# Kernel tuning notes

Hardware: AMD Instinct MI355X
Metric: run time of the kernel (lower is better)

## Reference

```python
import jax, jax.numpy as jnp
import numpy as np

INPUT_DIM = 512
SMOOTH_FACTOR = 1.0
NOISE_THRESHOLD = 0.0
TAIL_THRESHOLD = 0.45


def setup_inputs() -> dict:
    key = jax.random.key(0)
    k1, k2, k3, k4, k5 = jax.random.split(key, 5)
    B, T, D = 16, 4096, INPUT_DIM
    hidden = jax.random.normal(k1, (B, T, D), dtype=jnp.float32)
    mask = jnp.ones((B, 1, T), dtype=jnp.float32)
    # Conv1d(D, D, kernel=3) weight [out, in, k], Linear(D, 1) weight [1, D]
    conv_w = jax.random.normal(k2, (D, D, 3), dtype=jnp.float32) * (1.0 / np.sqrt(D * 3))
    conv_b = jax.random.normal(k3, (D,), dtype=jnp.float32) * 0.01
    out_w = jax.random.normal(k4, (1, D), dtype=jnp.float32) * (1.0 / np.sqrt(D))
    out_b = jax.random.normal(k5, (1,), dtype=jnp.float32) * 0.01
    return dict(hidden=hidden, mask=mask, conv_w=conv_w, conv_b=conv_b,
                out_w=out_w, out_b=out_b)


def _cif(hidden, alphas):
    """Vectorized continuous integrate-and-fire.
    hidden: [B, T1, D], alphas: [B, T1] -> padded frames [B, T1, D].
    Equivalent to the torch boolean-mask gather/roll/scatter version: for the
    k-th fire at time t_k, frame_k = Q[t_k] - Q[t_{k-1}] where
    Q[t] = cumsum(alpha*h)[t] - frac(cumsum(alpha))[t] * h[t].
    """
    B, T1, D = hidden.shape
    ps = jnp.cumsum(alphas, axis=1)                      # prefix sum of alphas
    psf = jnp.floor(ps)
    prev_psf = jnp.concatenate([jnp.zeros((B, 1), psf.dtype), psf[:, :-1]], axis=1)
    fire = (psf - prev_psf) > 0                          # [B, T1] bool, fire indicator
    frac = ps - psf                                      # remains at each position
    P = jnp.cumsum(alphas[..., None] * hidden, axis=1)   # [B, T1, D]
    Q = P - frac[..., None] * hidden                     # boundary-adjusted prefix
    k = jnp.cumsum(fire.astype(jnp.int32), axis=1) - 1   # fire ordinal per position
    idx = jnp.where(fire, k, T1)                         # dump non-fires to extra slot
    upd = jnp.where(fire[..., None], Q, 0.0)
    Qs = jnp.zeros((B, T1 + 1, D), hidden.dtype).at[jnp.arange(B)[:, None], idx].add(upd)[:, :T1]
    frames = Qs - jnp.concatenate([jnp.zeros((B, 1, D), hidden.dtype), Qs[:, :-1]], axis=1)
    batch_len = fire.sum(axis=1)                         # number of fires per batch
    valid = jnp.arange(T1)[None, :] < batch_len[:, None]
    return jnp.where(valid[..., None], frames, 0.0)


def reference(hidden, mask, conv_w, conv_b, out_w, out_b):
    B, T, D = hidden.shape
    # conv over time with pad (l_order=1, r_order=1), kernel 3, then ReLU
    x = jnp.transpose(hidden, (0, 2, 1))                 # [B, D, T]
    y = jax.lax.conv_general_dilated(x, conv_w, (1,), [(1, 1)],
                                     dimension_numbers=('NCH', 'OIH', 'NCH'))
    y = jax.nn.relu(y + conv_b[None, :, None])
    y = jnp.transpose(y, (0, 2, 1))                      # [B, T, D]
    o = y @ out_w.T + out_b                              # [B, T, 1]
    alphas = jax.nn.relu(jax.nn.sigmoid(o) * SMOOTH_FACTOR - NOISE_THRESHOLD)
    mk = jnp.transpose(mask, (0, 2, 1))                  # [B, T, 1]
    alphas = (alphas * mk)[..., 0]                       # [B, T]
    mk2 = mk[..., 0]                                     # [B, T]
    # tail_process_fn: add tail_threshold at first padded position
    zeros_t = jnp.zeros((B, 1), alphas.dtype)
    ones_t = jnp.ones((B, 1), alphas.dtype)
    mask_1 = jnp.concatenate([mk2, zeros_t], axis=1)     # [B, T+1]
    mask_2 = jnp.concatenate([ones_t, mk2], axis=1)
    tail = (mask_2 - mask_1) * TAIL_THRESHOLD
    alphas = jnp.concatenate([alphas, zeros_t], axis=1) + tail   # [B, T+1]
    h = jnp.concatenate([hidden, jnp.zeros((B, 1, D), hidden.dtype)], axis=1)
    token_num = jnp.floor(alphas.sum(-1))                # [B]
    acoustic = _cif(h, alphas)                           # [B, T+1, D] zero-padded
    # data-dependent truncation (eager, matches torch .item())
    token_num_int = int(np.asarray(jnp.max(token_num)).astype(np.int32))
    acoustic = acoustic[:, :token_num_int, :]
    return acoustic, token_num, alphas
```

## Files before the change

### kernel.cpp

```cpp
#include <hip/hip_runtime.h>
#include <math.h>

#define B_ 16
#define T_ 4096
#define D_ 512
#define T1_ 4097
#define NTHR 1024

#define SMOOTH_FACTOR 1.0
#define NOISE_THRESHOLD 0.0
#define TAIL_THRESHOLD 0.45

typedef short bf16x8 __attribute__((ext_vector_type(8)));
typedef float f32x16 __attribute__((ext_vector_type(16)));
union U4 { uint4 u; bf16x8 s; };

#define WB_OFF   ((size_t)0)
#define A64_OFF  ((size_t)3145728)
#define FT_OFF   ((size_t)3670144)
#define FF_OFF   ((size_t)3932352)
#define LEN_OFF  ((size_t)4456768)

__device__ __forceinline__ unsigned bf_rne(unsigned x) {
    return (x + 0x7FFFu + ((x >> 16) & 1u)) >> 16;
}

__global__ void k_wt(const float* __restrict__ cw, uint4* __restrict__ wb) {
    int idx = blockIdx.x * 256 + threadIdx.x;
    if (idx >= 196608) return;
    int o  = idx & 511;
    int r  = idx >> 9;
    int kg = r & 1;
    int rc = r >> 1;
    int comp = rc / 96;
    int c    = rc - comp * 96;
    unsigned uw[4];
    #pragma unroll
    for (int j = 0; j < 4; ++j) {
        unsigned short us[2];
        #pragma unroll
        for (int q = 0; q < 2; ++q) {
            int e = j * 2 + q;
            int k = c * 16 + kg * 8 + e;
            int tap = k >> 9, i = k & 511;
            float v = cw[((size_t)o * D_ + i) * 3 + tap];
            unsigned x  = __float_as_uint(v);
            unsigned hi = bf_rne(x);
            if (comp == 0) us[q] = (unsigned short)hi;
            else {
                float rem = v - __uint_as_float(hi << 16);
                us[q] = (unsigned short)bf_rne(__float_as_uint(rem));
            }
        }
        uw[j] = (unsigned)us[0] | ((unsigned)us[1] << 16);
    }
    wb[idx] = make_uint4(uw[0], uw[1], uw[2], uw[3]);
}

__global__ __launch_bounds__(NTHR)
void k_conv(const float* __restrict__ h, const uint4* __restrict__ wb,
            const float* __restrict__ cbp, const float* __restrict__ owp,
            const float* __restrict__ mask, const float* __restrict__ obp,
            float* __restrict__ out_alpha, double* __restrict__ a64) {
    extern __shared__ uint4 lds[];
    uint4* Ahi = lds;
    uint4* Ami = lds + 66 * 65;

    const int tid  = threadIdx.x;
    const int b    = blockIdx.y;
    const int t0   = blockIdx.x * 64;
    const int lane = tid & 63;
    const int w    = tid >> 6;
    const int l31  = lane & 31;
    const int kg   = lane >> 5;

    const float* hb = h + (size_t)b * T_ * D_;

    {
        float4 x0, x1, y0, y1;
        int idx = tid;
        if (idx < 4224) {
            int r = idx >> 6, cu4 = idx & 63, t = t0 - 1 + r;
            if (t >= 0 && t < T_) {
                const float* p = hb + (size_t)t * D_ + cu4 * 8;
                x0 = *(const float4*)p; x1 = *(const float4*)(p + 4);
            } else { x0 = x1 = make_float4(0.f, 0.f, 0.f, 0.f); }
        }
        for (int it = 0; it < 5; ++it) {
            int nidx = idx + 1024;
            if (it < 4 && nidx < 4224) {
                int r = nidx >> 6, cu4 = nidx & 63, t = t0 - 1 + r;
                if (t >= 0 && t < T_) {
                    const float* p = hb + (size_t)t * D_ + cu4 * 8;
                    y0 = *(const float4*)p; y1 = *(const float4*)(p + 4);
                } else { y0 = y1 = make_float4(0.f, 0.f, 0.f, 0.f); }
            }
            if (idx < 4224) {
                float v[8] = {x0.x, x0.y, x0.z, x0.w, x1.x, x1.y, x1.z, x1.w};
                unsigned hw[4], mw[4];
                #pragma unroll
                for (int j = 0; j < 4; ++j) {
                    unsigned short hs_[2], ms_[2];
                    #pragma unroll
                    for (int q = 0; q < 2; ++q) {
                        float f = v[j * 2 + q];
                        unsigned hi = bf_rne(__float_as_uint(f));
                        float rem = f - __uint_as_float(hi << 16);
                        hs_[q] = (unsigned short)hi;
                        ms_[q] = (unsigned short)bf_rne(__float_as_uint(rem));
                    }
                    hw[j] = hs_[0] | ((unsigned)hs_[1] << 16);
                    mw[j] = ms_[0] | ((unsigned)ms_[1] << 16);
                }
                int r = idx >> 6, cu4 = idx & 63;
                Ahi[r * 65 + cu4] = make_uint4(hw[0], hw[1], hw[2], hw[3]);
                Ami[r * 65 + cu4] = make_uint4(mw[0], mw[1], mw[2], mw[3]);
            }
            x0 = y0; x1 = y1; idx = nidx;
        }
    }
    __syncthreads();

    f32x16 acc0 = {0,0,0,0,0,0,0,0,0,0,0,0,0,0,0,0};
    f32x16 acc1 = acc0;

    const uint4* wph = wb + ((size_t)kg * 512 + w * 32 + l31);
    const uint4* wpm = wph + 98304;

    U4 whA, wmA, whB, wmB;
    U4 ah0A, am0A, ah1A, am1A, ah0B, am0B, ah1B, am1B;

    #define LOADW(Q, WH, WM) {                 \
        size_t c_ = (size_t)(Q) * 1024;        \
        WH.u = wph[c_];  WM.u = wpm[c_]; }

    #define LOADA(Q, AH0, AM0, AH1, AM1) {                              \
        int ia_ = (l31 + ((Q) >> 5)) * 65 + (((Q) & 31) << 1) + kg;     \
        AH0.u = Ahi[ia_];            AM0.u = Ami[ia_];                  \
        AH1.u = Ahi[ia_ + 32 * 65];  AM1.u = Ami[ia_ + 32 * 65]; }

    #define MF3(AH, AM, CC, WH, WM) {                                           \
        CC = __builtin_amdgcn_mfma_f32_32x32x16_bf16(AH.s, WH.s, CC, 0, 0, 0);  \
        CC = __builtin_amdgcn_mfma_f32_32x32x16_bf16(AH.s, WM.s, CC, 0, 0, 0);  \
        CC = __builtin_amdgcn_mfma_f32_32x32x16_bf16(AM.s, WH.s, CC, 0, 0, 0); }

    LOADW(0, whA, wmA);
    LOADW(1, whB, wmB);
    LOADA(0, ah0A, am0A, ah1A, am1A);

    for (int q = 0; q < 96; q += 2) {
        LOADA(q + 1, ah0B, am0B, ah1B, am1B);
        MF3(ah0A, am0A, acc0, whA, wmA);
        MF3(ah1A, am1A, acc1, whA, wmA);
        if (q + 2 < 96) {
            LOADW(q + 2, whA, wmA);
            LOADA(q + 2, ah0A, am0A, ah1A, am1A);
        }
        MF3(ah0B, am0B, acc0, whB, wmB);
        MF3(ah1B, am1B, acc1, whB, wmB);
        if (q + 3 < 96) LOADW(q + 3, whB, wmB);
    }
    #undef LOADW
    #undef LOADA
    #undef MF3

    const int o = w * 32 + l31;
    const double cbv = (double)cbp[o];
    const double owv = (double)owp[o];
    __syncthreads();
    double* pw = (double*)lds;

    #pragma unroll
    for (int s = 0; s < 2; ++s) {
        const f32x16 ac = s ? acc1 : acc0;
        #pragma unroll
        for (int v = 0; v < 16; ++v) {
            double z = (double)ac[v] + cbv;
            z = z > 0.0 ? z : 0.0;
            double p = owv * z;
            #pragma unroll
            for (int off = 1; off < 32; off <<= 1) p += __shfl_xor(p, off);
            if (l31 == 0) {
                int m = (v & 3) + 8 * (v >> 2) + 4 * kg;
                pw[w * 64 + s * 32 + m] = p;
            }
        }
    }
    __syncthreads();

    if (tid < 64) {
        int t = t0 + tid;
        double osum = (double)obp[0];
        #pragma unroll
        for (int j = 0; j < 16; ++j) osum += pw[j * 64 + tid];
        double sg = 1.0 / (1.0 + exp(-osum));
        double ap = sg * SMOOTH_FACTOR - NOISE_THRESHOLD;
        if (ap < 0.0) ap = 0.0;
        double mk = (double)mask[b * T_ + t];
        double mprev = (t == 0) ? 1.0 : (double)mask[b * T_ + t - 1];
        double a = ap * mk + TAIL_THRESHOLD * (mprev - mk);
        out_alpha[(size_t)b * T1_ + t] = (float)a;
        a64[(size_t)b * T1_ + t] = a;
    }
}

__global__ void k_scan(const double* __restrict__ a64, const float* __restrict__ mask,
                       float* __restrict__ out_tok, float* __restrict__ out_alpha,
                       int* __restrict__ fire_t, double* __restrict__ fire_frac,
                       int* __restrict__ blen) {
    const int b = blockIdx.x;
    const int lane = threadIdx.x;
    const double* ab = a64 + (size_t)b * T1_;
    double carry = 0.0;
    int nf = 0;

    double a = ab[lane];
    for (int c = 0; c < 65; ++c) {
        int t = c * 64 + lane;
        if (t == T_) {
            a = TAIL_THRESHOLD * (double)mask[b * T_ + T_ - 1];
            out_alpha[(size_t)b * T1_ + T_] = (float)a;
        } else if (t > T_) {
            a = 0.0;
        }
        int tn = t + 64;
        double anext = (tn < T_) ? ab[tn] : 0.0;
        double x = a;
        #pragma unroll
        for (int off = 1; off < 64; off <<= 1) {
            double y = __shfl_up(x, off);
            if (lane >= off) x += y;
        }
        double ps = carry + x;
        double ps_prev = __shfl_up(ps, 1);
        if (lane == 0) ps_prev = carry;
        double psf = floor(ps), ppsf = floor(ps_prev);
        bool fire = (t <= T_) && (psf > ppsf);
        unsigned long long m = __ballot(fire);
        if (fire) {
            int k = nf + (int)__popcll(m & ((1ull << lane) - 1ull));
            fire_t[(size_t)b * T1_ + k] = t;
            fire_frac[(size_t)b * T1_ + k] = ps - psf;
        }
        nf += (int)__popcll(m);
        carry = __shfl(ps, 63);
        a = anext;
    }
    if (lane == 0) {
        blen[b] = nf;
        out_tok[b] = (float)floor(carry);
    }
}

__global__ void k_frames(const float* __restrict__ h, const double* __restrict__ a64,
                         const int* __restrict__ fire_t, const double* __restrict__ fire_frac,
                         const int* __restrict__ blen, float* __restrict__ out, int K) {
    const int k = blockIdx.x;
    const int b = blockIdx.y;
    const int tid = threadIdx.x;
    double ax = 0.0, ay = 0.0, az = 0.0, aw = 0.0;
    const int len = blen[b];
    if (k < len) {
        const int t1 = fire_t[(size_t)b * T1_ + k];
        const int t0 = (k > 0) ? fire_t[(size_t)b * T1_ + k - 1] : -1;
        const double f1 = fire_frac[(size_t)b * T1_ + k];
        const double f0 = (k > 0) ? fire_frac[(size_t)b * T1_ + k - 1] : 0.0;
        if (t0 >= 0 && t0 < T_) {
            float4 hv = *(const float4*)(h + ((size_t)b * T_ + t0) * D_ + (tid << 2));
            ax = fma(f0, (double)hv.x, ax); ay = fma(f0, (double)hv.y, ay);
            az = fma(f0, (double)hv.z, az); aw = fma(f0, (double)hv.w, aw);
        }
        for (int t = t0 + 1; t <= t1; ++t) {
            if (t >= T_) break;
            double c = a64[(size_t)b * T1_ + t] - ((t == t1) ? f1 : 0.0);
            float4 hv = *(const float4*)(h + ((size_t)b * T_ + t) * D_ + (tid << 2));
            ax = fma(c, (double)hv.x, ax); ay = fma(c, (double)hv.y, ay);
            az = fma(c, (double)hv.z, az); aw = fma(c, (double)hv.w, aw);
        }
    }
    float4 o = make_float4((float)ax, (float)ay, (float)az, (float)aw);
    *(float4*)(out + ((size_t)b * K + k) * D_ + (tid << 2)) = o;
}

extern "C" void kernel_launch(void* const* d_in, const int* in_sizes, int n_in,
                              void* d_out, int out_size, void* d_ws, size_t ws_size,
                              hipStream_t stream) {
    const float* h    = (const float*)d_in[0];
    const float* mask = (const float*)d_in[1];
    const float* cw   = (const float*)d_in[2];
    const float* cb   = (const float*)d_in[3];
    const float* ow   = (const float*)d_in[4];
    const float* ob   = (const float*)d_in[5];

    char* ws = (char*)d_ws;
    uint4*  wb        = (uint4*)(ws + WB_OFF);
    double* a64       = (double*)(ws + A64_OFF);
    int*    fire_t    = (int*)(ws + FT_OFF);
    double* fire_frac = (double*)(ws + FF_OFF);
    int*    blen      = (int*)(ws + LEN_OFF);

    long long K = ((long long)out_size - B_ - (long long)B_ * T1_) / ((long long)B_ * D_);
    if (K < 1) K = 1;
    float* out_ac    = (float*)d_out;
    float* out_tok   = out_ac + (size_t)B_ * K * D_;
    float* out_alpha = out_tok + B_;

    const int lds = 2 * 66 * 65 * 16;
    (void)hipFuncSetAttribute((const void*)k_conv,
                              hipFuncAttributeMaxDynamicSharedMemorySize, lds);

    k_wt<<<dim3(768), dim3(256), 0, stream>>>(cw, wb);
    k_conv<<<dim3(T_ / 64, B_), dim3(NTHR), lds, stream>>>(h, wb, cb, ow, mask, ob,
                                                           out_alpha, a64);
    k_scan<<<dim3(B_), dim3(64), 0, stream>>>(a64, mask, out_tok, out_alpha,
                                              fire_t, fire_frac, blen);
    k_frames<<<dim3((unsigned)K, B_), dim3(128), 0, stream>>>(h, a64, fire_t, fire_frac,
                                                              blen, out_ac, (int)K);
}
```

Measured before the change: 416.6 us.

## Enlarge conv tile to 128 timesteps with 2x2 warp tiling and staged channel halves

Each conv block now covers 128 timesteps instead of 64. The 16 waves are arranged as 8 output groups by 2 time groups, and each wave computes a 2x2 set of 32x32 MFMA tiles, so every weight fragment loaded from global memory is reused across twice as many timesteps. To keep LDS usage unchanged, the input tile is staged in two halves of 256 channels, with a barrier between the phases. This lowers weight traffic and the number of blocks, but adds register pressure from four accumulators, an extra synchronisation, and the loss of overlap between input staging and compute.

```diff
diff --git a/kernel.cpp b/kernel.cpp
--- a/kernel.cpp
+++ b/kernel.cpp
@@ -64,135 +64,139 @@
             float* __restrict__ out_alpha, double* __restrict__ a64) {
     extern __shared__ uint4 lds[];
     uint4* Ahi = lds;
-    uint4* Ami = lds + 66 * 65;
+    uint4* Ami = lds + 130 * 33;
 
     const int tid  = threadIdx.x;
     const int b    = blockIdx.y;
-    const int t0   = blockIdx.x * 64;
+    const int t0   = blockIdx.x * 128;
     const int lane = tid & 63;
     const int w    = tid >> 6;
     const int l31  = lane & 31;
     const int kg   = lane >> 5;
+    const int og   = w >> 1;
+    const int tg   = w & 1;
 
     const float* hb = h + (size_t)b * T_ * D_;
 
-    {
-        float4 x0, x1, y0, y1;
-        int idx = tid;
-        if (idx < 4224) {
-            int r = idx >> 6, cu4 = idx & 63, t = t0 - 1 + r;
-            if (t >= 0 && t < T_) {
-                const float* p = hb + (size_t)t * D_ + cu4 * 8;
-                x0 = *(const float4*)p; x1 = *(const float4*)(p + 4);
-            } else { x0 = x1 = make_float4(0.f, 0.f, 0.f, 0.f); }
-        }
-        for (int it = 0; it < 5; ++it) {
-            int nidx = idx + 1024;
-            if (it < 4 && nidx < 4224) {
-                int r = nidx >> 6, cu4 = nidx & 63, t = t0 - 1 + r;
-                if (t >= 0 && t < T_) {
-                    const float* p = hb + (size_t)t * D_ + cu4 * 8;
-                    y0 = *(const float4*)p; y1 = *(const float4*)(p + 4);
-                } else { y0 = y1 = make_float4(0.f, 0.f, 0.f, 0.f); }
-            }
-            if (idx < 4224) {
-                float v[8] = {x0.x, x0.y, x0.z, x0.w, x1.x, x1.y, x1.z, x1.w};
-                unsigned hw[4], mw[4];
-                #pragma unroll
-                for (int j = 0; j < 4; ++j) {
-                    unsigned short hs_[2], ms_[2];
-                    #pragma unroll
-                    for (int q = 0; q < 2; ++q) {
-                        float f = v[j * 2 + q];
-                        unsigned hi = bf_rne(__float_as_uint(f));
-                        float rem = f - __uint_as_float(hi << 16);
-                        hs_[q] = (unsigned short)hi;
-                        ms_[q] = (unsigned short)bf_rne(__float_as_uint(rem));
-                    }
-                    hw[j] = hs_[0] | ((unsigned)hs_[1] << 16);
-                    mw[j] = ms_[0] | ((unsigned)ms_[1] << 16);
-                }
-                int r = idx >> 6, cu4 = idx & 63;
-                Ahi[r * 65 + cu4] = make_uint4(hw[0], hw[1], hw[2], hw[3]);
-                Ami[r * 65 + cu4] = make_uint4(mw[0], mw[1], mw[2], mw[3]);
-            }
-            x0 = y0; x1 = y1; idx = nidx;
-        }
-    }
-    __syncthreads();
-
-    f32x16 acc0 = {0,0,0,0,0,0,0,0,0,0,0,0,0,0,0,0};
-    f32x16 acc1 = acc0;
-
-    const uint4* wph = wb + ((size_t)kg * 512 + w * 32 + l31);
-    const uint4* wpm = wph + 98304;
-
-    U4 whA, wmA, whB, wmB;
-    U4 ah0A, am0A, ah1A, am1A, ah0B, am0B, ah1B, am1B;
-
-    #define LOADW(Q, WH, WM) {                 \
-        size_t c_ = (size_t)(Q) * 1024;        \
-        WH.u = wph[c_];  WM.u = wpm[c_]; }
-
-    #define LOADA(Q, AH0, AM0, AH1, AM1) {                              \
-        int ia_ = (l31 + ((Q) >> 5)) * 65 + (((Q) & 31) << 1) + kg;     \
-        AH0.u = Ahi[ia_];            AM0.u = Ami[ia_];                  \
-        AH1.u = Ahi[ia_ + 32 * 65];  AM1.u = Ami[ia_ + 32 * 65]; }
+    f32x16 c00 = {0,0,0,0,0,0,0,0,0,0,0,0,0,0,0,0};
+    f32x16 c01 = c00, c10 = c00, c11 = c00;
+
+    const uint4* wph0 = wb + ((size_t)kg * 512 + og * 64 + l31);
+    const uint4* wph1 = wph0 + 32;
+    const uint4* wpm0 = wph0 + 98304;
+    const uint4* wpm1 = wph1 + 98304;
+
+    U4 wAh0, wAh1, wAm0, wAm1, wBh0, wBh1, wBm0, wBm1;
+    U4 ah0, am0, ah1, am1;
+
+    #define GC(PH, Q) ((((Q) >> 4) << 5) + (PH) * 16 + ((Q) & 15))
+    #define LOADW(C, H0, H1, M0, M1) { size_t c_ = (size_t)(C) * 1024;  \
+        H0.u = wph0[c_]; H1.u = wph1[c_];                               \
+        M0.u = wpm0[c_]; M1.u = wpm1[c_]; }
+    #define LOADWG(PH, QQ, H0, H1, M0, M1) { int p_ = (PH), q_ = (QQ);  \
+        if (q_ >= 48) { p_++; q_ -= 48; }                               \
+        if (p_ < 2) LOADW(GC(p_, q_), H0, H1, M0, M1); }
+
+    #define LOADA(Q) {                                                          \
+        int ia_ = (tg * 64 + l31 + ((Q) >> 4)) * 33 + (((Q) & 15) << 1) + kg;   \
+        ah0.u = Ahi[ia_];            am0.u = Ami[ia_];                          \
+        ah1.u = Ahi[ia_ + 32 * 33];  am1.u = Ami[ia_ + 32 * 33]; }
 
     #define MF3(AH, AM, CC, WH, WM) {                                           \
         CC = __builtin_amdgcn_mfma_f32_32x32x16_bf16(AH.s, WH.s, CC, 0, 0, 0);  \
         CC = __builtin_amdgcn_mfma_f32_32x32x16_bf16(AH.s, WM.s, CC, 0, 0, 0);  \
         CC = __builtin_amdgcn_mfma_f32_32x32x16_bf16(AM.s, WH.s, CC, 0, 0, 0); }
 
-    LOADW(0, whA, wmA);
-    LOADW(1, whB, wmB);
-    LOADA(0, ah0A, am0A, ah1A, am1A);
-
-    for (int q = 0; q < 96; q += 2) {
-        LOADA(q + 1, ah0B, am0B, ah1B, am1B);
-        MF3(ah0A, am0A, acc0, whA, wmA);
-        MF3(ah1A, am1A, acc1, whA, wmA);
-        if (q + 2 < 96) {
-            LOADW(q + 2, whA, wmA);
-            LOADA(q + 2, ah0A, am0A, ah1A, am1A);
-        }
-        MF3(ah0B, am0B, acc0, whB, wmB);
-        MF3(ah1B, am1B, acc1, whB, wmB);
-        if (q + 3 < 96) LOADW(q + 3, whB, wmB);
-    }
+    #define MFMA12(H0, H1, M0, M1) {      \
+        MF3(ah0, am0, c00, H0, M0);       \
+        MF3(ah0, am0, c01, H1, M1);       \
+        MF3(ah1, am1, c10, H0, M0);       \
+        MF3(ah1, am1, c11, H1, M1); }
+
+    LOADWG(0, 0, wAh0, wAh1, wAm0, wAm1);
+    LOADWG(0, 1, wBh0, wBh1, wBm0, wBm1);
+
+    for (int ph = 0; ph < 2; ++ph) {
+        if (ph) __syncthreads();
+        for (int idx = tid; idx < 4160; idx += NTHR) {
+            int r = idx >> 5, cu4 = idx & 31, t = t0 - 1 + r;
+            float v[8];
+            if (t >= 0 && t < T_) {
+                const float* p = hb + (size_t)t * D_ + ph * 256 + cu4 * 8;
+                float4 x0 = *(const float4*)p;
+                float4 x1 = *(const float4*)(p + 4);
+                v[0]=x0.x; v[1]=x0.y; v[2]=x0.z; v[3]=x0.w;
+                v[4]=x1.x; v[5]=x1.y; v[6]=x1.z; v[7]=x1.w;
+            } else {
+                #pragma unroll
+                for (int j = 0; j < 8; ++j) v[j] = 0.f;
+            }
+            unsigned hw[4], mw[4];
+            #pragma unroll
+            for (int j = 0; j < 4; ++j) {
+                unsigned short hs_[2], ms_[2];
+                #pragma unroll
+                for (int q = 0; q < 2; ++q) {
+                    float f = v[j * 2 + q];
+                    unsigned hi = bf_rne(__float_as_uint(f));
+                    float rem = f - __uint_as_float(hi << 16);
+                    hs_[q] = (unsigned short)hi;
+                    ms_[q] = (unsigned short)bf_rne(__float_as_uint(rem));
+                }
+                hw[j] = hs_[0] | ((unsigned)hs_[1] << 16);
+                mw[j] = ms_[0] | ((unsigned)ms_[1] << 16);
+            }
+            Ahi[r * 33 + cu4] = make_uint4(hw[0], hw[1], hw[2], hw[3]);
+            Ami[r * 33 + cu4] = make_uint4(mw[0], mw[1], mw[2], mw[3]);
+        }
+        __syncthreads();
+
+        for (int q = 0; q < 48; q += 2) {
+            LOADA(q);
+            MFMA12(wAh0, wAh1, wAm0, wAm1);
+            LOADWG(ph, q + 2, wAh0, wAh1, wAm0, wAm1);
+            LOADA(q + 1);
+            MFMA12(wBh0, wBh1, wBm0, wBm1);
+            LOADWG(ph, q + 3, wBh0, wBh1, wBm0, wBm1);
+        }
+    }
+    #undef GC
     #undef LOADW
+    #undef LOADWG
     #undef LOADA
     #undef MF3
-
-    const int o = w * 32 + l31;
-    const double cbv = (double)cbp[o];
-    const double owv = (double)owp[o];
+    #undef MFMA12
+
+    const int o0 = og * 64 + l31, o1 = o0 + 32;
+    const double cb0 = (double)cbp[o0], cb1 = (double)cbp[o1];
+    const double ow0 = (double)owp[o0], ow1 = (double)owp[o1];
     __syncthreads();
     double* pw = (double*)lds;
 
     #pragma unroll
     for (int s = 0; s < 2; ++s) {
-        const f32x16 ac = s ? acc1 : acc0;
+        const f32x16 aa = s ? c10 : c00;
+        const f32x16 ab = s ? c11 : c01;
         #pragma unroll
         for (int v = 0; v < 16; ++v) {
-            double z = (double)ac[v] + cbv;
-            z = z > 0.0 ? z : 0.0;
-            double p = owv * z;
+            double z0 = (double)aa[v] + cb0; z0 = z0 > 0.0 ? z0 : 0.0;
+            double z1 = (double)ab[v] + cb1; z1 = z1 > 0.0 ? z1 : 0.0;
+            double p = fma(ow0, z0, ow1 * z1);
             #pragma unroll
             for (int off = 1; off < 32; off <<= 1) p += __shfl_xor(p, off);
             if (l31 == 0) {
                 int m = (v & 3) + 8 * (v >> 2) + 4 * kg;
-                pw[w * 64 + s * 32 + m] = p;
+                pw[og * 128 + tg * 64 + s * 32 + m] = p;
             }
         }
     }
     __syncthreads();
 
-    if (tid < 64) {
+    if (tid < 128) {
         int t = t0 + tid;
         double osum = (double)obp[0];
         #pragma unroll
-        for (int j = 0; j < 16; ++j) osum += pw[j * 64 + tid];
+        for (int j = 0; j < 8; ++j) osum += pw[j * 128 + tid];
         double sg = 1.0 / (1.0 + exp(-osum));
         double ap = sg * SMOOTH_FACTOR - NOISE_THRESHOLD;
         if (ap < 0.0) ap = 0.0;
@@ -305,13 +309,13 @@
     float* out_tok   = out_ac + (size_t)B_ * K * D_;
     float* out_alpha = out_tok + B_;
 
-    const int lds = 2 * 66 * 65 * 16;
+    const int lds = 2 * 130 * 33 * 16;
     (void)hipFuncSetAttribute((const void*)k_conv,
                               hipFuncAttributeMaxDynamicSharedMemorySize, lds);
 
     k_wt<<<dim3(768), dim3(256), 0, stream>>>(cw, wb);
-    k_conv<<<dim3(T_ / 64, B_), dim3(NTHR), lds, stream>>>(h, wb, cb, ow, mask, ob,
-                                                           out_alpha, a64);
+    k_conv<<<dim3(T_ / 128, B_), dim3(NTHR), lds, stream>>>(h, wb, cb, ow, mask, ob,
+                                                            out_alpha, a64);
     k_scan<<<dim3(B_), dim3(64), 0, stream>>>(a64, mask, out_tok, out_alpha,
                                               fire_t, fire_frac, blen);
     k_frames<<<dim3((unsigned)K, B_), dim3(128), 0, stream>>>(h, a64, fire_t, fire_frac,
```

After: 355.1 us. 1.17x faster.
